# Performance work log

Measured on AMD Instinct MI355X. Metric: run time of the kernel, lower is better.

Reference implementation:

```python
import jax, jax.numpy as jnp
import numpy as np

# Arbitrary non-contiguous kernel tap offsets (constructor arg sk_ind)
SK_IND = np.array([-512, -256, -128, -96, -64, -48, -32, -24, -16, -12, -8, -6,
                   -4, -3, -2, -1, 0, 1, 2, 3, 4, 6, 8, 12, 16, 24, 32, 48,
                   64, 96, 128, 256], dtype=np.int32)
IN_CHANNELS = 64
OUT_CHANNELS = 64
BATCH = 16
INPUT_LEN = 4096


def setup_inputs() -> dict:
    key = jax.random.key(0)
    k1, k2 = jax.random.split(key)
    x = jax.random.normal(k1, (BATCH, IN_CHANNELS, INPUT_LEN), dtype=jnp.float32)
    sk_weights = jax.random.normal(k2, (OUT_CHANNELS, IN_CHANNELS, SK_IND.shape[0]), dtype=jnp.float32)
    return {"x": x, "sk_weights": sk_weights}


def reference(x, sk_weights):
    # x: [B, Cin, L]; sk_weights: [Cout, Cin, K]
    B, C, L = x.shape
    low_pad = max(-int(SK_IND.min()), 0)   # zeros consumed by negative taps
    high_pad = max(int(SK_IND.max()), 0)   # zeros consumed by positive taps
    # Original pads zeros AFTER the signal: [x, zeros(high_pad), zeros(low_pad)];
    # negative numpy indices then wrap into the trailing low_pad zeros.
    padded = jnp.concatenate([x, jnp.zeros((B, C, high_pad + low_pad), x.dtype)], axis=-1)
    padded_len = L + high_pad + low_pad
    idx = SK_IND[:, None] + np.arange(L)                 # [K, L], static
    idx = np.where(idx < 0, padded_len + idx, idx)       # emulate numpy negative-index wrap
    gathered = padded[:, :, idx]                          # [B, Cin, K, L]
    # Per-position GEMM: contract over (Cin, K)
    return jnp.einsum('oik,bikl->bol', sk_weights, gathered)  # [B, Cout, L]
```

## Files before the change

kernel.cpp:

```cpp
#include <hip/hip_runtime.h>


#define B_    16
#define CIN   64
#define COUT  64
#define LEN   4096
#define NTAP  32

typedef float f32x4 __attribute__((ext_vector_type(4)));
typedef short bf16x8_s __attribute__((ext_vector_type(8)));
typedef __bf16 bf16x8_b __attribute__((ext_vector_type(8)));

template <typename V>
static __device__ inline auto mfma_16x16x32_bf16(V a, V b, f32x4 c, int)
    -> decltype(__builtin_amdgcn_mfma_f32_16x16x32_bf16(a, b, c, 0, 0, 0)) {
  return __builtin_amdgcn_mfma_f32_16x16x32_bf16(a, b, c, 0, 0, 0);
}
template <typename V>
static __device__ inline f32x4 mfma_16x16x32_bf16(V a, V b, f32x4 c, long) {
  return __builtin_amdgcn_mfma_f32_16x16x32_bf16(
      __builtin_bit_cast(bf16x8_b, a), __builtin_bit_cast(bf16x8_b, b), c, 0, 0, 0);
}

static __device__ inline unsigned short f32_to_bf16_rne(float f) {
  unsigned int u = __builtin_bit_cast(unsigned int, f);
  u += 0x7fffu + ((u >> 16) & 1u);
  return (unsigned short)(u >> 16);
}

__global__ __launch_bounds__(256) void prep_w(const float* __restrict__ w,
                                              unsigned short* __restrict__ wf) {
  const int base = blockIdx.x * 1024;
#pragma unroll
  for (int it = 0; it < 4; ++it) {
    const int e = base + it * 256 + threadIdx.x;
    const int j = e & 7;
    const int lane = (e >> 3) & 63;
    const int m = (e >> 9) & 3;
    const int c = (e >> 11) & 1;
    const int t = e >> 12;
    const int o = m * 16 + (lane & 15);
    const int i = c * 32 + (lane >> 4) * 8 + j;
    wf[e] = f32_to_bf16_rne(w[(size_t)(o * CIN + i) * NTAP + t]);
  }
}

__global__ __launch_bounds__(512, 2) void sconv_main(const float* __restrict__ x,
                                                     const unsigned short* __restrict__ wf,
                                                     float* __restrict__ out) {
  constexpr int TAP[NTAP] = {-512, -256, -128, -96, -64, -48, -32, -24, -16, -12, -8,
                             -6,   -4,   -3,   -2,  -1,  0,   1,   2,   3,   4,  6,
                             8,    12,   16,   24,  32,  48,  64,  96,  128, 256};
  __shared__ alignas(16) char smem[131072];

  const int id = blockIdx.x;
  const int b = (id & 7) * 2 + (id >> 7);
  const int l0 = ((id >> 3) & 15) * 256;
  const int lb = l0 + 512;
  const int tid = threadIdx.x;
  const int wv = tid >> 6, lane = tid & 63;
  const int q = lane >> 4, r = lane & 15;
  const int lh = wv >> 1, ch = wv & 1;

  const char* wbase = (const char*)wf;
  const float* xb = x + (size_t)b * CIN * LEN;

  auto stage_iter = [&](int lc) {
    const int h = lane & 7;
    const int i0 = 16 * (wv & 3) + 2 * h;
    const int row0 = lc + ((wv >> 2) << 5) + ((lane >> 3) << 2);
    const int gl = l0 + row0;
    f32x4 va = {0.f, 0.f, 0.f, 0.f}, vb = {0.f, 0.f, 0.f, 0.f};
    if ((unsigned)gl < (unsigned)LEN) {
      va = *(const f32x4*)&xb[(size_t)i0 * LEN + gl];
      vb = *(const f32x4*)&xb[(size_t)(i0 + 1) * LEN + gl];
    }
#pragma unroll
    for (int j = 0; j < 4; ++j) {
      const unsigned u = (unsigned)f32_to_bf16_rne(va[j]) |
                         ((unsigned)f32_to_bf16_rne(vb[j]) << 16);
      const int slot = (lb + row0 + j) & 1023;
      const int cs = (i0 >> 3) ^ (slot & 7);
      *(unsigned*)(smem + slot * 128 + (cs << 4) + (i0 & 7) * 2) = u;
    }
  };

  bf16x8_s Wreg[2][4], Breg[2][4];
  f32x4 acc[4][4] = {};

  auto loadW = [&](int tt, int p) {
    const char* src = wbase + tt * 8192 + ch * 4096 + lane * 16;
#pragma unroll
    for (int m = 0; m < 4; ++m)
      Wreg[p][m] = *(const bf16x8_s*)(src + m * 1024);
  };
  auto readB = [&](int tt, int p) {
    const int e = (TAP[tt] + r) & 7;
#pragma unroll
    for (int n = 0; n < 4; ++n) {
      const int slot = (lb + TAP[tt] + lh * 64 + 16 * n + r) & 1023;
      Breg[p][n] = *(const bf16x8_s*)(smem + slot * 128 + (((ch * 4 + q) ^ e) << 4));
    }
  };

  loadW(0, 0);
#pragma unroll 4
  for (int k = 0; k < 12; ++k) stage_iter(-512 + k * 64);
  __syncthreads();
  readB(0, 0);

#pragma unroll
  for (int t = 0; t < NTAP; ++t) {
    const int p = t & 1;
    if (t < 4) stage_iter(256 + t * 64);
    if (t == 6) __syncthreads();
    if (t + 1 < NTAP) {
      loadW(t + 1, p ^ 1);
      readB(t + 1, p ^ 1);
    }
    __builtin_amdgcn_sched_barrier(0);
#pragma unroll
    for (int m = 0; m < 4; ++m)
#pragma unroll
      for (int n = 0; n < 4; ++n)
        acc[m][n] = mfma_16x16x32_bf16(Wreg[p][m], Breg[p][n], acc[m][n], 0);
  }

  __syncthreads();
  if (ch == 1) {
#pragma unroll
    for (int m = 0; m < 4; ++m)
#pragma unroll
      for (int n = 0; n < 4; ++n)
        *(f32x4*)(smem + lh * 16384 + ((m * 4 + n) * 64 + lane) * 16) = acc[m][n];
  }
  __syncthreads();
  if (ch == 0) {
#pragma unroll
    for (int m = 0; m < 4; ++m)
#pragma unroll
      for (int n = 0; n < 4; ++n) {
        const f32x4 other = *(const f32x4*)(smem + lh * 16384 + ((m * 4 + n) * 64 + lane) * 16);
        const f32x4 v = acc[m][n] + other;
#pragma unroll
        for (int d = 0; d < 4; ++d) {
          const int o = 16 * m + 4 * q + d;
          const int l = l0 + lh * 64 + 16 * n + r;
          out[((size_t)b * COUT + o) * LEN + l] = v[d];
        }
      }
  }
}

extern "C" void kernel_launch(void* const* d_in, const int* in_sizes, int n_in,
                              void* d_out, int out_size, void* d_ws, size_t ws_size,
                              hipStream_t stream) {
  const float* x = (const float*)d_in[0];
  const float* w = (const float*)d_in[1];
  float* out = (float*)d_out;

  unsigned short* wfp = (unsigned short*)d_ws;

  prep_w<<<dim3(128), 256, 0, stream>>>(w, wfp);
  sconv_main<<<dim3(256), 512, 0, stream>>>(x, wfp, out);
}
```

Measured before the change: 89.36 us.

## Reorder taps to start with near window and overlap far-tap staging with MFMA

Taps are now processed in an order that begins with the small offsets, so the prologue stages only the window around the output tile. The far negative and positive regions are staged after each MFMA batch during the first ten taps, with a barrier before the far taps are read. The cross-wave reduction in the epilogue is split so both channel-halves each store half and sum/write half, balancing the final work. The change shortens the serial prologue and overlaps global loads with compute, at the cost of more complex ordering and a mid-loop barrier.

```diff
diff --git a/kernel.cpp b/kernel.cpp
--- a/kernel.cpp
+++ b/kernel.cpp
@@ -51,6 +51,10 @@
   constexpr int TAP[NTAP] = {-512, -256, -128, -96, -64, -48, -32, -24, -16, -12, -8,
                              -6,   -4,   -3,   -2,  -1,  0,   1,   2,   3,   4,  6,
                              8,    12,   16,   24,  32,  48,  64,  96,  128, 256};
+  constexpr int ORD[NTAP] = {10, 11, 12, 13, 14, 15, 16, 17, 18, 19, 20, 21, 22,
+                             0,  1,  2,  3,  4,  5,  6,  7,  8,  9,
+                             23, 24, 25, 26, 27, 28, 29, 30, 31};
+  constexpr int P2[10] = {-128, -192, -256, -320, -384, -448, -512, 320, 384, 448};
   __shared__ alignas(16) char smem[131072];
 
   const int id = blockIdx.x;
@@ -103,20 +107,26 @@
     }
   };
 
-  loadW(0, 0);
-#pragma unroll 4
-  for (int k = 0; k < 12; ++k) stage_iter(-512 + k * 64);
+  loadW(ORD[0], 0);
+  stage_iter(0);
+  stage_iter(64);
+  stage_iter(128);
+  stage_iter(192);
+  stage_iter(256);
+  stage_iter(-64);
   __syncthreads();
-  readB(0, 0);
+  readB(ORD[0], 0);
 
 #pragma unroll
-  for (int t = 0; t < NTAP; ++t) {
-    const int p = t & 1;
-    if (t < 4) stage_iter(256 + t * 64);
-    if (t == 6) __syncthreads();
-    if (t + 1 < NTAP) {
-      loadW(t + 1, p ^ 1);
-      readB(t + 1, p ^ 1);
+  for (int j = 0; j < NTAP; ++j) {
+    const int p = j & 1;
+    if (j == 13) {
+      __syncthreads();
+      readB(ORD[13], p);
+    }
+    if (j + 1 < NTAP) {
+      loadW(ORD[j + 1], p ^ 1);
+      if (j != 12) readB(ORD[j + 1], p ^ 1);
     }
     __builtin_amdgcn_sched_barrier(0);
 #pragma unroll
@@ -124,27 +134,35 @@
 #pragma unroll
       for (int n = 0; n < 4; ++n)
         acc[m][n] = mfma_16x16x32_bf16(Wreg[p][m], Breg[p][n], acc[m][n], 0);
+    __builtin_amdgcn_sched_barrier(0);
+    if (j < 10) stage_iter(P2[j]);
   }
 
   __syncthreads();
-  if (ch == 1) {
+  {
+    const int mstore = (ch == 0) ? 2 : 0;
+    const int sstore = (ch == 0) ? 16384 : 0;
 #pragma unroll
-    for (int m = 0; m < 4; ++m)
+    for (int mm = 0; mm < 2; ++mm)
 #pragma unroll
       for (int n = 0; n < 4; ++n)
-        *(f32x4*)(smem + lh * 16384 + ((m * 4 + n) * 64 + lane) * 16) = acc[m][n];
+        *(f32x4*)(smem + lh * 32768 + sstore + ((mm * 4 + n) * 64 + lane) * 16) =
+            acc[mstore + mm][n];
   }
   __syncthreads();
-  if (ch == 0) {
+  {
+    const int mout = (ch == 0) ? 0 : 2;
+    const int sread = (ch == 0) ? 0 : 16384;
 #pragma unroll
-    for (int m = 0; m < 4; ++m)
+    for (int mm = 0; mm < 2; ++mm)
 #pragma unroll
       for (int n = 0; n < 4; ++n) {
-        const f32x4 other = *(const f32x4*)(smem + lh * 16384 + ((m * 4 + n) * 64 + lane) * 16);
-        const f32x4 v = acc[m][n] + other;
+        const f32x4 other =
+            *(const f32x4*)(smem + lh * 32768 + sread + ((mm * 4 + n) * 64 + lane) * 16);
+        const f32x4 v = acc[mout + mm][n] + other;
 #pragma unroll
         for (int d = 0; d < 4; ++d) {
-          const int o = 16 * m + 4 * q + d;
+          const int o = 16 * (mout + mm) + 4 * q + d;
           const int l = l0 + lh * 64 + 16 * n + r;
           out[((size_t)b * COUT + o) * LEN + l] = v[d];
         }
```

Measured after the change: 216.9 us. 143% more time.
